# Performance work log

Hardware: AMD Instinct MI355X
Metric: run time of the kernel (lower is better)

Reference implementation:

```python
import jax, jax.numpy as jnp
import numpy as np

N, E, C = 50000, 300000, 256  # nodes, edges, hidden size


def setup_inputs() -> dict:
    key = jax.random.key(0)
    ks = jax.random.split(key, 12)
    s = 0.05  # param init scale
    return {
        "x": jax.random.normal(ks[0], (N, C), dtype=jnp.float32),
        "edge_index": jax.random.randint(ks[1], (2, E), 0, N, dtype=jnp.int32),
        # GATConv layer 1 (heads=1): shared lin weight, att_src/att_dst vectors, bias
        "W1": jax.random.normal(ks[2], (C, C), dtype=jnp.float32) * s,
        "a1_src": jax.random.normal(ks[3], (C,), dtype=jnp.float32) * s,
        "a1_dst": jax.random.normal(ks[4], (C,), dtype=jnp.float32) * s,
        "b1": jnp.zeros((C,), dtype=jnp.float32),
        # GATConv layer 2
        "W2": jax.random.normal(ks[5], (C, C), dtype=jnp.float32) * s,
        "a2_src": jax.random.normal(ks[6], (C,), dtype=jnp.float32) * s,
        "a2_dst": jax.random.normal(ks[7], (C,), dtype=jnp.float32) * s,
        "b2": jnp.zeros((C,), dtype=jnp.float32),
        # Final Linear (torch convention: W [out, in], y = x @ W.T + b)
        "Wl": jax.random.normal(ks[8], (C, C), dtype=jnp.float32) * s,
        "bl": jnp.zeros((C,), dtype=jnp.float32),
    }


def _gat_conv(x, src, dst, W, a_src, a_dst, b):
    # PyG GATConv, heads=1, negative_slope=0.2, self-loops already appended.
    h = x @ W                                  # [N, C]
    alpha_src = h @ a_src                      # [N]
    alpha_dst = h @ a_dst                      # [N]
    e = jax.nn.leaky_relu(alpha_src[src] + alpha_dst[dst], 0.2)   # [E']
    # numerically stable softmax over incoming edges of each destination node
    m = jax.ops.segment_max(e, dst, num_segments=N)               # [N]
    ex = jnp.exp(e - m[dst])
    den = jax.ops.segment_sum(ex, dst, num_segments=N)            # [N]
    w = ex / den[dst]                                              # [E']
    out = jax.ops.segment_sum(h[src] * w[:, None], dst, num_segments=N)  # [N, C]
    return out + b


def reference(x, edge_index, W1, a1_src, a1_dst, b1, W2, a2_src, a2_dst, b2, Wl, bl):
    # add_self_loops (done inside each GATConv in PyG; appending once to the
    # input edge list is equivalent since both convs see the same edges)
    loops = jnp.arange(N, dtype=edge_index.dtype)
    ei = jnp.concatenate([edge_index, jnp.stack([loops, loops])], axis=1)
    src, dst = ei[0], ei[1]
    x = jax.nn.relu(_gat_conv(x, src, dst, W1, a1_src, a1_dst, b1))
    x = jax.nn.relu(_gat_conv(x, src, dst, W2, a2_src, a2_dst, b2))
    return x @ Wl.T + bl
```

## Files before the change

kernel.cpp:

```cpp
#include <hip/hip_runtime.h>

#define NN 50000
#define EE 300000
#define ET (EE + NN)
#define CD 256
#define PAD_M 50176
#define NB 196

typedef unsigned short ushortT;
typedef short bf16x8 __attribute__((ext_vector_type(8)));
typedef float f32x4 __attribute__((ext_vector_type(4)));

__device__ __forceinline__ ushortT f2b(float f) {
    unsigned u = __builtin_bit_cast(unsigned, f);
    unsigned r = (u + 0x7FFFu + ((u >> 16) & 1u)) >> 16;
    return (ushortT)r;
}
__device__ __forceinline__ float b2f(ushortT b) {
    return __builtin_bit_cast(float, ((unsigned)b) << 16);
}

#define PREP_X 12500
#define PREP_W1 12564
#define PREP_W2 12628
#define PREP_WL 12692
#define PREP_END 12888

__global__ __launch_bounds__(256) void prep_kernel(
    const float* __restrict__ x, const float* __restrict__ W1,
    const float* __restrict__ W2, const float* __restrict__ Wl,
    ushortT* __restrict__ B0, ushortT* __restrict__ W1t,
    ushortT* __restrict__ W2t, ushortT* __restrict__ Wlt,
    int* __restrict__ deg, float* __restrict__ asA, float* __restrict__ adA,
    float* __restrict__ asB, float* __restrict__ adB) {
    __shared__ float t[32][33];
    int b = blockIdx.x, tidx = threadIdx.x;
    if (b < PREP_X) {
        int id = b * 256 + tidx;
        float4 v = *(const float4*)(x + (size_t)id * 4);
        ushort4 o;
        o.x = f2b(v.x); o.y = f2b(v.y); o.z = f2b(v.z); o.w = f2b(v.w);
        *(ushort4*)(B0 + (size_t)id * 4) = o;
    } else if (b < PREP_W2) {
        const float* W = (b < PREP_W1) ? W1 : W2;
        ushortT* Bt = (b < PREP_W1) ? W1t : W2t;
        int rel = b - ((b < PREP_W1) ? PREP_X : PREP_W1);
        int bx = (rel & 7) * 32;
        int by = (rel >> 3) * 32;
        int xx = tidx & 31, yy = tidx >> 5;
        for (int y = yy; y < 32; y += 8) t[y][xx] = W[(size_t)(bx + y) * CD + by + xx];
        __syncthreads();
        for (int y = yy; y < 32; y += 8)
            Bt[(size_t)(by + y) * CD + bx + xx] = f2b(t[xx][y]);
    } else if (b < PREP_WL) {
        int id = (b - PREP_W2) * 256 + tidx;
        float4 v = *(const float4*)(Wl + (size_t)id * 4);
        ushort4 o;
        o.x = f2b(v.x); o.y = f2b(v.y); o.z = f2b(v.z); o.w = f2b(v.w);
        *(ushort4*)(Wlt + (size_t)id * 4) = o;
    } else {
        int i = (b - PREP_WL) * 256 + tidx;
        if (i < NN) {
            deg[i] = 1;
            asA[i] = 0.f; adA[i] = 0.f;
            asB[i] = 0.f; adB[i] = 0.f;
        }
    }
}


__global__ void count_deg_kernel(const int* __restrict__ ei, int* __restrict__ deg) {
    int i = blockIdx.x * blockDim.x + threadIdx.x;
    if (i < EE) atomicAdd(&deg[ei[EE + i]], 1);
}

__global__ __launch_bounds__(256) void scan_part(const int* __restrict__ deg,
                                                 int* __restrict__ bsum) {
    int i = blockIdx.x * 256 + threadIdx.x;
    int v = (i < NN) ? deg[i] : 0;
#pragma unroll
    for (int off = 32; off > 0; off >>= 1) v += __shfl_down(v, off);
    __shared__ int w[4];
    if ((threadIdx.x & 63) == 0) w[threadIdx.x >> 6] = v;
    __syncthreads();
    if (threadIdx.x == 0) bsum[blockIdx.x] = w[0] + w[1] + w[2] + w[3];
}

__global__ __launch_bounds__(256) void scan_fill(const int* __restrict__ deg,
                                                 const int* __restrict__ bsum,
                                                 int* __restrict__ row_start,
                                                 int* __restrict__ fill_pos) {
    __shared__ int s[256];
    int t = threadIdx.x;
    int bv = (t < NB) ? bsum[t] : 0;
    s[t] = bv;
    __syncthreads();
    for (int off = 1; off < 256; off <<= 1) {
        int x = s[t];
        int y = (t >= off) ? s[t - off] : 0;
        __syncthreads();
        s[t] = x + y;
        __syncthreads();
    }
    int boff = s[blockIdx.x] - bsum[blockIdx.x];
    __syncthreads();
    int i = blockIdx.x * 256 + t;
    int v = (i < NN) ? deg[i] : 0;
    s[t] = v;
    __syncthreads();
    for (int off = 1; off < 256; off <<= 1) {
        int x = s[t];
        int y = (t >= off) ? s[t - off] : 0;
        __syncthreads();
        s[t] = x + y;
        __syncthreads();
    }
    int excl = s[t] - v + boff;
    if (i < NN) {
        row_start[i] = excl;
        fill_pos[i] = excl;
    }
    if (blockIdx.x == 0 && t == 0) row_start[NN] = ET;
}

__global__ void fill_csr_kernel(const int* __restrict__ ei, int* __restrict__ fill_pos,
                                int* __restrict__ srcs) {
    int i = blockIdx.x * blockDim.x + threadIdx.x;
    if (i < EE) {
        int s = ei[i];
        int d = ei[EE + i];
        int p = atomicAdd(&fill_pos[d], 1);
        srcs[p] = s;
    } else if (i < ET) {
        int n = i - EE;
        int p = atomicAdd(&fill_pos[n], 1);
        srcs[p] = n;
    }
}


template <int OUTF32, int ALPHA>
__global__ __launch_bounds__(256, 4) void gemm_mfma(const ushortT* __restrict__ A,
                                                    const ushortT* __restrict__ Bt,
                                                    const float* __restrict__ bias,
                                                    float* __restrict__ outF,
                                                    ushortT* __restrict__ outB,
                                                    const float* __restrict__ a_src,
                                                    const float* __restrict__ a_dst,
                                                    float* __restrict__ as_g,
                                                    float* __restrict__ ad_g,
                                                    int M) {
    __shared__ ushortT Bs[64 * 256];
    int tid = threadIdx.x;
    int wave = tid >> 6, lane = tid & 63;
    int wm = wave * 32;
    int id = blockIdx.x;
    int bm = (id >> 2) * 128, bn = (id & 3) * 64;
    int l15 = lane & 15, quad = lane >> 4;

#pragma unroll
    for (int p = 0; p < 8; ++p) {
        int c = p * 256 + tid;
        int slot = c >> 5;
        int piece = c & 31;
        int col = (slot & 15) * 4 + (slot >> 4);
        int spiece = piece ^ (slot & 31);
        const ushortT* gb = Bt + (size_t)(bn + col) * CD + spiece * 8;
        __builtin_amdgcn_global_load_lds(
            (const __attribute__((address_space(1))) void*)gb,
            (__attribute__((address_space(3))) void*)(Bs + (size_t)(p * 256 + wave * 64) * 8),
            16, 0, 0);
    }

    bf16x8 a[2][8];
#pragma unroll
    for (int kk = 0; kk < 8; ++kk)
#pragma unroll
        for (int i = 0; i < 2; ++i)
            a[i][kk] = *(const bf16x8*)(A + (size_t)(bm + wm + i * 16 + l15) * CD + kk * 32 + quad * 8);

    __syncthreads();

    f32x4 acc[2][4] = {};

#pragma unroll
    for (int kk = 0; kk < 8; ++kk) {
        bf16x8 b[4];
        int kc = kk * 4 + quad;
#pragma unroll
        for (int j = 0; j < 4; ++j) {
            int slot = j * 16 + l15;
            b[j] = *(const bf16x8*)(Bs + (size_t)slot * 256 + (size_t)(kc ^ (slot & 31)) * 8);
        }
#pragma unroll
        for (int i = 0; i < 2; ++i)
#pragma unroll
            for (int j = 0; j < 4; ++j)
                acc[i][j] = __builtin_amdgcn_mfma_f32_16x16x32_bf16(a[i][kk], b[j], acc[i][j], 0, 0, 0);
    }

    int colb = bn + l15 * 4;
#pragma unroll
    for (int i = 0; i < 2; ++i) {
#pragma unroll
        for (int r = 0; r < 4; ++r) {
            int row = bm + wm + i * 16 + quad * 4 + r;
            if (OUTF32) {
                if (row < M) {
                    float4 bv = *(const float4*)(bias + colb);
                    float4 v;
                    v.x = acc[i][0][r] + bv.x;
                    v.y = acc[i][1][r] + bv.y;
                    v.z = acc[i][2][r] + bv.z;
                    v.w = acc[i][3][r] + bv.w;
                    *(float4*)(outF + (size_t)row * CD + colb) = v;
                }
            } else {
                ushort4 o;
                o.x = f2b(acc[i][0][r]);
                o.y = f2b(acc[i][1][r]);
                o.z = f2b(acc[i][2][r]);
                o.w = f2b(acc[i][3][r]);
                *(ushort4*)(outB + (size_t)row * CD + colb) = o;
            }
        }
    }

    if (ALPHA) {
        float4 avs = *(const float4*)(a_src + colb);
        float4 avd = *(const float4*)(a_dst + colb);
#pragma unroll
        for (int i = 0; i < 2; ++i) {
#pragma unroll
            for (int r = 0; r < 4; ++r) {
                int row = bm + wm + i * 16 + quad * 4 + r;
                float ps = acc[i][0][r] * avs.x + acc[i][1][r] * avs.y +
                           acc[i][2][r] * avs.z + acc[i][3][r] * avs.w;
                float pd = acc[i][0][r] * avd.x + acc[i][1][r] * avd.y +
                           acc[i][2][r] * avd.z + acc[i][3][r] * avd.w;
#pragma unroll
                for (int off = 1; off < 16; off <<= 1) {
                    ps += __shfl_xor(ps, off);
                    pd += __shfl_xor(pd, off);
                }
                if (l15 == 0 && row < M) {
                    atomicAdd(&as_g[row], ps);
                    atomicAdd(&ad_g[row], pd);
                }
            }
        }
    }
}


__device__ __forceinline__ float lrelu02(float x) { return x > 0.f ? x : 0.2f * x; }

__global__ __launch_bounds__(256) void gat_agg(const ushortT* __restrict__ h,
                                               const float* __restrict__ as_,
                                               const float* __restrict__ ad_,
                                               const int* __restrict__ row_start,
                                               const int* __restrict__ srcs,
                                               const float* __restrict__ bias,
                                               ushortT* __restrict__ out) {
    int node = blockIdx.x * 4 + (threadIdx.x >> 6);
    int lane = threadIdx.x & 63;
    if (node >= NN) return;
    int rs = row_start[node];
    int re = row_start[node + 1];
    int deg = re - rs;
    float adst = ad_[node];

    float a0 = 0.f, a1 = 0.f, a2 = 0.f, a3 = 0.f;

    if (deg <= 64) {
        int s_lane = srcs[rs + ((lane < deg) ? lane : 0)];
        float e = (lane < deg) ? lrelu02(as_[s_lane] + adst) : -1e30f;
        float m = e;
#pragma unroll
        for (int off = 1; off < 64; off <<= 1) m = fmaxf(m, __shfl_xor(m, off));
        float ex = (lane < deg) ? __expf(e - m) : 0.f;
        float den = ex;
#pragma unroll
        for (int off = 1; off < 64; off <<= 1) den += __shfl_xor(den, off);
        float wl = ex / den;

        for (int kk = 0; kk < deg; kk += 8) {
            int s[8];
            float w[8];
#pragma unroll
            for (int t = 0; t < 8; ++t) {
                int idx = kk + t;
                int ii = (idx < deg) ? idx : kk;
                int sv = __shfl(s_lane, ii);
                float wv = __shfl(wl, ii);
                s[t] = sv;
                w[t] = (idx < deg) ? wv : 0.f;
            }
            ushort4 hv[8];
#pragma unroll
            for (int t = 0; t < 8; ++t)
                hv[t] = *(const ushort4*)(h + (size_t)s[t] * CD + lane * 4);
#pragma unroll
            for (int t = 0; t < 8; ++t) {
                a0 += w[t] * b2f(hv[t].x);
                a1 += w[t] * b2f(hv[t].y);
                a2 += w[t] * b2f(hv[t].z);
                a3 += w[t] * b2f(hv[t].w);
            }
        }
    } else {
        float m = -1e30f;
        for (int k = rs + lane; k < re; k += 64) {
            float e = lrelu02(as_[srcs[k]] + adst);
            m = fmaxf(m, e);
        }
#pragma unroll
        for (int off = 1; off < 64; off <<= 1) m = fmaxf(m, __shfl_xor(m, off));
        float den = 0.f;
        for (int k = rs + lane; k < re; k += 64) {
            float e = lrelu02(as_[srcs[k]] + adst);
            den += __expf(e - m);
        }
#pragma unroll
        for (int off = 1; off < 64; off <<= 1) den += __shfl_xor(den, off);
        float inv_den = 1.f / den;
        for (int k = rs; k < re; ++k) {
            int s = srcs[k];
            float e = lrelu02(as_[s] + adst);
            float w = __expf(e - m) * inv_den;
            ushort4 hv = *(const ushort4*)(h + (size_t)s * CD + lane * 4);
            a0 += w * b2f(hv.x);
            a1 += w * b2f(hv.y);
            a2 += w * b2f(hv.z);
            a3 += w * b2f(hv.w);
        }
    }

    float4 b4 = *(const float4*)(bias + lane * 4);
    a0 = fmaxf(a0 + b4.x, 0.f);
    a1 = fmaxf(a1 + b4.y, 0.f);
    a2 = fmaxf(a2 + b4.z, 0.f);
    a3 = fmaxf(a3 + b4.w, 0.f);
    ushort4 o;
    o.x = f2b(a0);
    o.y = f2b(a1);
    o.z = f2b(a2);
    o.w = f2b(a3);
    *(ushort4*)(out + (size_t)node * CD + lane * 4) = o;
}


extern "C" void kernel_launch(void* const* d_in, const int* in_sizes, int n_in,
                              void* d_out, int out_size, void* d_ws, size_t ws_size,
                              hipStream_t stream) {
    const float* x = (const float*)d_in[0];
    const int* ei = (const int*)d_in[1];
    const float* W1 = (const float*)d_in[2];
    const float* a1s = (const float*)d_in[3];
    const float* a1d = (const float*)d_in[4];
    const float* b1 = (const float*)d_in[5];
    const float* W2 = (const float*)d_in[6];
    const float* a2s = (const float*)d_in[7];
    const float* a2d = (const float*)d_in[8];
    const float* b2 = (const float*)d_in[9];
    const float* Wl = (const float*)d_in[10];
    const float* bl = (const float*)d_in[11];
    float* out = (float*)d_out;

    char* w = (char*)d_ws;
    ushortT* B0 = (ushortT*)w; w += (size_t)PAD_M * CD * 2;
    ushortT* B1 = (ushortT*)w; w += (size_t)PAD_M * CD * 2;
    ushortT* B2 = (ushortT*)w; w += (size_t)PAD_M * CD * 2;
    ushortT* W1t = (ushortT*)w; w += (size_t)CD * CD * 2;
    ushortT* W2t = (ushortT*)w; w += (size_t)CD * CD * 2;
    ushortT* Wlt = (ushortT*)w; w += (size_t)CD * CD * 2;
    float* asA = (float*)w; w += (size_t)NN * 4;
    float* adA = (float*)w; w += (size_t)NN * 4;
    float* asB = (float*)w; w += (size_t)NN * 4;
    float* adB = (float*)w; w += (size_t)NN * 4;
    int* deg = (int*)w; w += (size_t)NN * 4;
    int* fill_pos = (int*)w; w += (size_t)NN * 4;
    int* srcs = (int*)w; w += (size_t)ET * 4;
    int* bsum = (int*)w; w += 1024;
    int* row_start = (int*)w; w += (size_t)(NN + 1) * 4;

    prep_kernel<<<PREP_END, 256, 0, stream>>>(x, W1, W2, Wl, B0, W1t, W2t, Wlt,
                                              deg, asA, adA, asB, adB);

    count_deg_kernel<<<(EE + 255) / 256, 256, 0, stream>>>(ei, deg);
    scan_part<<<NB, 256, 0, stream>>>(deg, bsum);
    scan_fill<<<NB, 256, 0, stream>>>(deg, bsum, row_start, fill_pos);
    fill_csr_kernel<<<(ET + 255) / 256, 256, 0, stream>>>(ei, fill_pos, srcs);

    int ggrid = (PAD_M / 128) * 4;
    int nwave_blocks = (NN + 3) / 4;

    gemm_mfma<0, 1><<<ggrid, 256, 0, stream>>>(B0, W1t, nullptr, nullptr, B1,
                                               a1s, a1d, asA, adA, NN);
    gat_agg<<<nwave_blocks, 256, 0, stream>>>(B1, asA, adA, row_start, srcs, b1, B2);

    gemm_mfma<0, 1><<<ggrid, 256, 0, stream>>>(B2, W2t, nullptr, nullptr, B1,
                                               a2s, a2d, asB, adB, NN);
    gat_agg<<<nwave_blocks, 256, 0, stream>>>(B1, asB, adB, row_start, srcs, b2, B0);

    gemm_mfma<1, 0><<<ggrid, 256, 0, stream>>>(B0, Wlt, bl, out, nullptr,
                                               nullptr, nullptr, nullptr, nullptr, NN);
}
```

Baseline: 295.1 us.

## Precompute W·a attention vectors and fold alpha dot products into prep/aggregation

Uses the identity (xW)·a = x·(Wa) to precompute per-layer attention vectors with a small kernel. The alpha_src/alpha_dst scores are then computed from the layer input: in the prep kernel for layer 1 and in the aggregation epilogue for layer 2. This removes the atomicAdd-based alpha reduction from the GEMM epilogue and the zero-initialization of those buffers. It adds one tiny kernel launch, and because the scores now come from fp32 inputs rather than bf16 GEMM outputs, results change slightly.

```diff
diff --git a/kernel.cpp b/kernel.cpp
--- a/kernel.cpp
+++ b/kernel.cpp
@@ -20,6 +20,37 @@
     return __builtin_bit_cast(float, ((unsigned)b) << 16);
 }
 
+
+__global__ __launch_bounds__(256) void wvec_kernel(
+    const float* __restrict__ W1, const float* __restrict__ a1s,
+    const float* __restrict__ a1d, const float* __restrict__ W2,
+    const float* __restrict__ a2s, const float* __restrict__ a2d,
+    float* __restrict__ w1s, float* __restrict__ w1d,
+    float* __restrict__ w2s, float* __restrict__ w2d) {
+    int b = blockIdx.x;
+    const float* W = (b < 64) ? W1 : W2;
+    const float* vs = (b < 64) ? a1s : a2s;
+    const float* vd = (b < 64) ? a1d : a2d;
+    float* os = (b < 64) ? w1s : w2s;
+    float* od = (b < 64) ? w1d : w2d;
+    int r = (b & 63) * 4 + (threadIdx.x >> 6);
+    int lane = threadIdx.x & 63;
+    float4 wv = *(const float4*)(W + (size_t)r * CD + lane * 4);
+    float4 s4 = *(const float4*)(vs + lane * 4);
+    float4 d4 = *(const float4*)(vd + lane * 4);
+    float ss = wv.x * s4.x + wv.y * s4.y + wv.z * s4.z + wv.w * s4.w;
+    float dd = wv.x * d4.x + wv.y * d4.y + wv.z * d4.z + wv.w * d4.w;
+#pragma unroll
+    for (int off = 1; off < 64; off <<= 1) {
+        ss += __shfl_xor(ss, off);
+        dd += __shfl_xor(dd, off);
+    }
+    if (lane == 0) {
+        os[r] = ss;
+        od[r] = dd;
+    }
+}
+
 #define PREP_X 12500
 #define PREP_W1 12564
 #define PREP_W2 12628
@@ -31,16 +62,31 @@
     const float* __restrict__ W2, const float* __restrict__ Wl,
     ushortT* __restrict__ B0, ushortT* __restrict__ W1t,
     ushortT* __restrict__ W2t, ushortT* __restrict__ Wlt,
-    int* __restrict__ deg, float* __restrict__ asA, float* __restrict__ adA,
-    float* __restrict__ asB, float* __restrict__ adB) {
+    int* __restrict__ deg, const float* __restrict__ w1s,
+    const float* __restrict__ w1d, float* __restrict__ as1,
+    float* __restrict__ ad1) {
     __shared__ float t[32][33];
     int b = blockIdx.x, tidx = threadIdx.x;
     if (b < PREP_X) {
-        int id = b * 256 + tidx;
-        float4 v = *(const float4*)(x + (size_t)id * 4);
+        int node = b * 4 + (tidx >> 6);
+        int lane = tidx & 63;
+        float4 v = *(const float4*)(x + (size_t)node * CD + lane * 4);
         ushort4 o;
         o.x = f2b(v.x); o.y = f2b(v.y); o.z = f2b(v.z); o.w = f2b(v.w);
-        *(ushort4*)(B0 + (size_t)id * 4) = o;
+        *(ushort4*)(B0 + (size_t)node * CD + lane * 4) = o;
+        float4 s4 = *(const float4*)(w1s + lane * 4);
+        float4 d4 = *(const float4*)(w1d + lane * 4);
+        float ss = v.x * s4.x + v.y * s4.y + v.z * s4.z + v.w * s4.w;
+        float dd = v.x * d4.x + v.y * d4.y + v.z * d4.z + v.w * d4.w;
+#pragma unroll
+        for (int off = 1; off < 64; off <<= 1) {
+            ss += __shfl_xor(ss, off);
+            dd += __shfl_xor(dd, off);
+        }
+        if (lane == 0) {
+            as1[node] = ss;
+            ad1[node] = dd;
+        }
     } else if (b < PREP_W2) {
         const float* W = (b < PREP_W1) ? W1 : W2;
         ushortT* Bt = (b < PREP_W1) ? W1t : W2t;
@@ -60,11 +106,7 @@
         *(ushort4*)(Wlt + (size_t)id * 4) = o;
     } else {
         int i = (b - PREP_WL) * 256 + tidx;
-        if (i < NN) {
-            deg[i] = 1;
-            asA[i] = 0.f; adA[i] = 0.f;
-            asB[i] = 0.f; adB[i] = 0.f;
-        }
+        if (i < NN) deg[i] = 1;
     }
 }
 
@@ -139,16 +181,12 @@
 }
 
 
-template <int OUTF32, int ALPHA>
+template <int OUTF32>
 __global__ __launch_bounds__(256, 4) void gemm_mfma(const ushortT* __restrict__ A,
                                                     const ushortT* __restrict__ Bt,
                                                     const float* __restrict__ bias,
                                                     float* __restrict__ outF,
                                                     ushortT* __restrict__ outB,
-                                                    const float* __restrict__ a_src,
-                                                    const float* __restrict__ a_dst,
-                                                    float* __restrict__ as_g,
-                                                    float* __restrict__ ad_g,
                                                     int M) {
     __shared__ ushortT Bs[64 * 256];
     int tid = threadIdx.x;
@@ -225,43 +263,23 @@
             }
         }
     }
-
-    if (ALPHA) {
-        float4 avs = *(const float4*)(a_src + colb);
-        float4 avd = *(const float4*)(a_dst + colb);
-#pragma unroll
-        for (int i = 0; i < 2; ++i) {
-#pragma unroll
-            for (int r = 0; r < 4; ++r) {
-                int row = bm + wm + i * 16 + quad * 4 + r;
-                float ps = acc[i][0][r] * avs.x + acc[i][1][r] * avs.y +
-                           acc[i][2][r] * avs.z + acc[i][3][r] * avs.w;
-                float pd = acc[i][0][r] * avd.x + acc[i][1][r] * avd.y +
-                           acc[i][2][r] * avd.z + acc[i][3][r] * avd.w;
-#pragma unroll
-                for (int off = 1; off < 16; off <<= 1) {
-                    ps += __shfl_xor(ps, off);
-                    pd += __shfl_xor(pd, off);
-                }
-                if (l15 == 0 && row < M) {
-                    atomicAdd(&as_g[row], ps);
-                    atomicAdd(&ad_g[row], pd);
-                }
-            }
-        }
-    }
 }
 
 
 __device__ __forceinline__ float lrelu02(float x) { return x > 0.f ? x : 0.2f * x; }
 
+template <int ALPHA2>
 __global__ __launch_bounds__(256) void gat_agg(const ushortT* __restrict__ h,
                                                const float* __restrict__ as_,
                                                const float* __restrict__ ad_,
                                                const int* __restrict__ row_start,
                                                const int* __restrict__ srcs,
                                                const float* __restrict__ bias,
-                                               ushortT* __restrict__ out) {
+                                               ushortT* __restrict__ out,
+                                               const float* __restrict__ w2s,
+                                               const float* __restrict__ w2d,
+                                               float* __restrict__ as_n,
+                                               float* __restrict__ ad_n) {
     int node = blockIdx.x * 4 + (threadIdx.x >> 6);
     int lane = threadIdx.x & 63;
     if (node >= NN) return;
@@ -347,6 +365,22 @@
     o.z = f2b(a2);
     o.w = f2b(a3);
     *(ushort4*)(out + (size_t)node * CD + lane * 4) = o;
+
+    if (ALPHA2) {
+        float4 s4 = *(const float4*)(w2s + lane * 4);
+        float4 d4 = *(const float4*)(w2d + lane * 4);
+        float ss = a0 * s4.x + a1 * s4.y + a2 * s4.z + a3 * s4.w;
+        float dd = a0 * d4.x + a1 * d4.y + a2 * d4.z + a3 * d4.w;
+#pragma unroll
+        for (int off = 1; off < 64; off <<= 1) {
+            ss += __shfl_xor(ss, off);
+            dd += __shfl_xor(dd, off);
+        }
+        if (lane == 0) {
+            as_n[node] = ss;
+            ad_n[node] = dd;
+        }
+    }
 }
 
 
@@ -374,18 +408,25 @@
     ushortT* W1t = (ushortT*)w; w += (size_t)CD * CD * 2;
     ushortT* W2t = (ushortT*)w; w += (size_t)CD * CD * 2;
     ushortT* Wlt = (ushortT*)w; w += (size_t)CD * CD * 2;
-    float* asA = (float*)w; w += (size_t)NN * 4;
-    float* adA = (float*)w; w += (size_t)NN * 4;
-    float* asB = (float*)w; w += (size_t)NN * 4;
-    float* adB = (float*)w; w += (size_t)NN * 4;
+    float* as1 = (float*)w; w += (size_t)NN * 4;
+    float* ad1 = (float*)w; w += (size_t)NN * 4;
+    float* as2 = (float*)w; w += (size_t)NN * 4;
+    float* ad2 = (float*)w; w += (size_t)NN * 4;
+    float* w1s = (float*)w; w += CD * 4;
+    float* w1d = (float*)w; w += CD * 4;
+    float* w2s = (float*)w; w += CD * 4;
+    float* w2d = (float*)w; w += CD * 4;
     int* deg = (int*)w; w += (size_t)NN * 4;
     int* fill_pos = (int*)w; w += (size_t)NN * 4;
     int* srcs = (int*)w; w += (size_t)ET * 4;
     int* bsum = (int*)w; w += 1024;
     int* row_start = (int*)w; w += (size_t)(NN + 1) * 4;
 
+    wvec_kernel<<<128, 256, 0, stream>>>(W1, a1s, a1d, W2, a2s, a2d,
+                                         w1s, w1d, w2s, w2d);
+
     prep_kernel<<<PREP_END, 256, 0, stream>>>(x, W1, W2, Wl, B0, W1t, W2t, Wlt,
-                                              deg, asA, adA, asB, adB);
+                                              deg, w1s, w1d, as1, ad1);
 
     count_deg_kernel<<<(EE + 255) / 256, 256, 0, stream>>>(ei, deg);
     scan_part<<<NB, 256, 0, stream>>>(deg, bsum);
@@ -395,14 +436,14 @@
     int ggrid = (PAD_M / 128) * 4;
     int nwave_blocks = (NN + 3) / 4;
 
-    gemm_mfma<0, 1><<<ggrid, 256, 0, stream>>>(B0, W1t, nullptr, nullptr, B1,
-                                               a1s, a1d, asA, adA, NN);
-    gat_agg<<<nwave_blocks, 256, 0, stream>>>(B1, asA, adA, row_start, srcs, b1, B2);
-
-    gemm_mfma<0, 1><<<ggrid, 256, 0, stream>>>(B2, W2t, nullptr, nullptr, B1,
-                                               a2s, a2d, asB, adB, NN);
-    gat_agg<<<nwave_blocks, 256, 0, stream>>>(B1, asB, adB, row_start, srcs, b2, B0);
-
-    gemm_mfma<1, 0><<<ggrid, 256, 0, stream>>>(B0, Wlt, bl, out, nullptr,
-                                               nullptr, nullptr, nullptr, nullptr, NN);
-}
+    gemm_mfma<0><<<ggrid, 256, 0, stream>>>(B0, W1t, nullptr, nullptr, B1, NN);
+    gat_agg<1><<<nwave_blocks, 256, 0, stream>>>(B1, as1, ad1, row_start, srcs,
+                                                 b1, B2, w2s, w2d, as2, ad2);
+
+    gemm_mfma<0><<<ggrid, 256, 0, stream>>>(B2, W2t, nullptr, nullptr, B1, NN);
+    gat_agg<0><<<nwave_blocks, 256, 0, stream>>>(B1, as2, ad2, row_start, srcs,
+                                                 b2, B0, nullptr, nullptr,
+                                                 nullptr, nullptr);
+
+    gemm_mfma<1><<<ggrid, 256, 0, stream>>>(B0, Wlt, bl, out, nullptr, NN);
+}
```

New measurement: 294.6 us. Within noise of the previous version (-0.2%).
